# Kernel tuning notes

Hardware: AMD Instinct MI355X
Metric: run time of the kernel (lower is better)

The kernel has to match this reference:

```python
import jax, jax.numpy as jnp
import numpy as np
from functools import partial

V_TH = 1.0
V_RESET = 0.0
ALPHA = 2.0
PI_H = 1.5707963267948966  # pi/2


@jax.custom_vjp
def _spike(v):
    # Heaviside spike with arctan surrogate gradient
    return (v >= V_TH).astype(v.dtype)


def _spike_fwd(v):
    return _spike(v), v - V_TH  # save h = v - V_TH


def _spike_bwd(h, g):
    pah = PI_H * ALPHA * h
    sg = ALPHA / (2.0 * (1.0 + pah * pah))
    return (g * sg,)


_spike.defvjp(_spike_fwd, _spike_bwd)


def _lif_dual(x, decay):
    # x: [T, B, N, C]; decay: [1] broadcast over all elements
    d = decay[0]

    def step(v, xt):
        v = d * v + xt                      # charge: [B, N, C]
        vpool = jnp.mean(v, axis=1)         # spatial mean -> [B, C] (pre-reset v)
        s = _spike(v)
        sr = jax.lax.stop_gradient(s)       # detach_reset=True
        v = (1.0 - sr) * v + sr * V_RESET   # hard reset
        return v, (s, vpool)

    v0 = jnp.zeros_like(x[0])
    _, (spikes, vpool) = jax.lax.scan(step, v0, x)
    return spikes, vpool                    # [T,B,N,C], [T,B,C]


def setup_inputs() -> dict:
    key = jax.random.key(0)
    T, B, N, C = 16, 32, 196, 512
    x = jax.random.normal(key, (T, B, N, C), dtype=jnp.float32)
    # decay = 1 - sigmoid(-log(tau-1)) = 1 - 1/tau = 0.5 for tau=2
    decay = jnp.full((1,), 0.5, dtype=jnp.float32)
    return {"x": x, "decay": decay}


def reference(x, decay):
    return _lif_dual(x, decay)
```

## Files before the change

kernel.cpp:

```cpp
#include <hip/hip_runtime.h>

constexpr int T   = 16;
constexpr int B   = 32;
constexpr int N   = 196;
constexpr int C   = 512;
constexpr int C4  = C / 4;
constexpr int TX  = 64;
constexpr int TY  = 4;
constexpr int RPT = 7;
constexpr int NCHUNK = N / (TY * RPT);
constexpr int CCHUNK = C4 / TX;

__global__ __launch_bounds__(TX * TY) void lif_dual_kernel(
    const float4* __restrict__ x,
    const float*  __restrict__ decay,
    float4* __restrict__ spikes,
    float*  __restrict__ vpool) {
  __shared__ float4 red[TY][4][TX];

  const int tx = threadIdx.x;
  const int ty = threadIdx.y;
  const int cc = blockIdx.x;
  const int nc = blockIdx.y;
  const int b  = blockIdx.z;

  const int c4    = cc * TX + tx;
  const int nbase = nc * (TY * RPT) + ty * RPT;

  const float d     = decay[0];
  const float inv_n = 1.0f / (float)N;

  float4 vpsum[T];
#pragma unroll
  for (int t = 0; t < T; ++t) vpsum[t] = make_float4(0.f, 0.f, 0.f, 0.f);

  const size_t tstride = (size_t)B * N * C4;

#pragma unroll 1
  for (int r = 0; r < RPT; ++r) {
    const int n = nbase + r;
    size_t idx = ((size_t)b * N + n) * C4 + c4;
    float4 v = make_float4(0.f, 0.f, 0.f, 0.f);

#pragma unroll
    for (int t = 0; t < T; ++t) {
      float4 xt = x[idx];

      v.x = d * v.x + xt.x;
      v.y = d * v.y + xt.y;
      v.z = d * v.z + xt.z;
      v.w = d * v.w + xt.w;

      vpsum[t].x += v.x;
      vpsum[t].y += v.y;
      vpsum[t].z += v.z;
      vpsum[t].w += v.w;

      float4 s;
      s.x = (v.x >= 1.0f) ? 1.0f : 0.0f;  v.x = (v.x >= 1.0f) ? 0.0f : v.x;
      s.y = (v.y >= 1.0f) ? 1.0f : 0.0f;  v.y = (v.y >= 1.0f) ? 0.0f : v.y;
      s.z = (v.z >= 1.0f) ? 1.0f : 0.0f;  v.z = (v.z >= 1.0f) ? 0.0f : v.z;
      s.w = (v.w >= 1.0f) ? 1.0f : 0.0f;  v.w = (v.w >= 1.0f) ? 0.0f : v.w;

      spikes[idx] = s;
      idx += tstride;
    }
  }

#pragma unroll 1
  for (int tc = 0; tc < T; tc += 4) {
#pragma unroll
    for (int j = 0; j < 4; ++j) red[ty][j][tx] = vpsum[tc + j];
    __syncthreads();

    float4 a0 = red[0][ty][tx];
    float4 a1 = red[1][ty][tx];
    float4 a2 = red[2][ty][tx];
    float4 a3 = red[3][ty][tx];
    float4 s;
    s.x = (a0.x + a1.x + a2.x + a3.x) * inv_n;
    s.y = (a0.y + a1.y + a2.y + a3.y) * inv_n;
    s.z = (a0.z + a1.z + a2.z + a3.z) * inv_n;
    s.w = (a0.w + a1.w + a2.w + a3.w) * inv_n;

    const int t = tc + ty;
    float* out = vpool + ((size_t)t * B + b) * C + (size_t)c4 * 4;
    atomicAdd(out + 0, s.x);
    atomicAdd(out + 1, s.y);
    atomicAdd(out + 2, s.z);
    atomicAdd(out + 3, s.w);
    __syncthreads();
  }
}

extern "C" void kernel_launch(void* const* d_in, const int* in_sizes, int n_in,
                              void* d_out, int out_size, void* d_ws, size_t ws_size,
                              hipStream_t stream) {
  const float4* x     = (const float4*)d_in[0];
  const float*  decay = (const float*)d_in[1];

  float* out = (float*)d_out;
  const size_t spike_elems = (size_t)T * B * N * C;
  const size_t vpool_elems = (size_t)T * B * C;

  float4* spikes = (float4*)out;
  float*  vpool  = out + spike_elems;

  hipMemsetAsync(vpool, 0, vpool_elems * sizeof(float), stream);

  dim3 block(TX, TY);
  dim3 grid(CCHUNK, NCHUNK, B);
  lif_dual_kernel<<<grid, block, 0, stream>>>(x, decay, spikes, vpool);
}
```

Measured before the change: 391.5 us.

## Replace atomic vpool reduction with partial-sum buffer and second reduction kernel

The float atomicAdd accumulation into vpool (and its memset) is replaced by per-chunk partial sums written to workspace, then reduced by a separate stage-2 kernel. The block shape also changes from 4x7 to 7x2 rows, giving more blocks and threads. Spike outputs are written with nontemporal stores so the large streaming output does not pollute cache. The cost is an extra kernel launch plus workspace traffic for the partial sums, and the result depends on the workspace being large enough.

```diff
diff --git a/kernel.cpp b/kernel.cpp
--- a/kernel.cpp
+++ b/kernel.cpp
@@ -6,16 +6,20 @@
 constexpr int C   = 512;
 constexpr int C4  = C / 4;
 constexpr int TX  = 64;
-constexpr int TY  = 4;
-constexpr int RPT = 7;
-constexpr int NCHUNK = N / (TY * RPT);
+constexpr int TY  = 7;
+constexpr int RPT = 2;
+constexpr int ROWS_PER_BLOCK = TY * RPT;
+constexpr int NCHUNK = N / ROWS_PER_BLOCK;
 constexpr int CCHUNK = C4 / TX;
+constexpr int PCHUNK_F4 = T * B * C4;
 
-__global__ __launch_bounds__(TX * TY) void lif_dual_kernel(
+typedef float f32x4 __attribute__((ext_vector_type(4)));
+
+__global__ __launch_bounds__(TX * TY) void lif_stage1(
     const float4* __restrict__ x,
     const float*  __restrict__ decay,
     float4* __restrict__ spikes,
-    float*  __restrict__ vpool) {
+    float4* __restrict__ partial) {
   __shared__ float4 red[TY][4][TX];
 
   const int tx = threadIdx.x;
@@ -24,11 +28,8 @@
   const int nc = blockIdx.y;
   const int b  = blockIdx.z;
 
-  const int c4    = cc * TX + tx;
-  const int nbase = nc * (TY * RPT) + ty * RPT;
-
-  const float d     = decay[0];
-  const float inv_n = 1.0f / (float)N;
+  const int c4 = cc * TX + tx;
+  const float d = decay[0];
 
   float4 vpsum[T];
 #pragma unroll
@@ -36,9 +37,9 @@
 
   const size_t tstride = (size_t)B * N * C4;
 
-#pragma unroll 1
+#pragma unroll
   for (int r = 0; r < RPT; ++r) {
-    const int n = nbase + r;
+    const int n = nc * ROWS_PER_BLOCK + ty * RPT + r;
     size_t idx = ((size_t)b * N + n) * C4 + c4;
     float4 v = make_float4(0.f, 0.f, 0.f, 0.f);
 
@@ -56,41 +57,54 @@
       vpsum[t].z += v.z;
       vpsum[t].w += v.w;
 
-      float4 s;
+      f32x4 s;
       s.x = (v.x >= 1.0f) ? 1.0f : 0.0f;  v.x = (v.x >= 1.0f) ? 0.0f : v.x;
       s.y = (v.y >= 1.0f) ? 1.0f : 0.0f;  v.y = (v.y >= 1.0f) ? 0.0f : v.y;
       s.z = (v.z >= 1.0f) ? 1.0f : 0.0f;  v.z = (v.z >= 1.0f) ? 0.0f : v.z;
       s.w = (v.w >= 1.0f) ? 1.0f : 0.0f;  v.w = (v.w >= 1.0f) ? 0.0f : v.w;
 
-      spikes[idx] = s;
+      __builtin_nontemporal_store(s, (f32x4*)&spikes[idx]);
       idx += tstride;
     }
   }
 
+  const int flat = ty * TX + tx;
 #pragma unroll 1
   for (int tc = 0; tc < T; tc += 4) {
 #pragma unroll
     for (int j = 0; j < 4; ++j) red[ty][j][tx] = vpsum[tc + j];
     __syncthreads();
-
-    float4 a0 = red[0][ty][tx];
-    float4 a1 = red[1][ty][tx];
-    float4 a2 = red[2][ty][tx];
-    float4 a3 = red[3][ty][tx];
-    float4 s;
-    s.x = (a0.x + a1.x + a2.x + a3.x) * inv_n;
-    s.y = (a0.y + a1.y + a2.y + a3.y) * inv_n;
-    s.z = (a0.z + a1.z + a2.z + a3.z) * inv_n;
-    s.w = (a0.w + a1.w + a2.w + a3.w) * inv_n;
-
-    const int t = tc + ty;
-    float* out = vpool + ((size_t)t * B + b) * C + (size_t)c4 * 4;
-    atomicAdd(out + 0, s.x);
-    atomicAdd(out + 1, s.y);
-    atomicAdd(out + 2, s.z);
-    atomicAdd(out + 3, s.w);
+    if (flat < 4 * TX) {
+      const int j   = flat >> 6;
+      const int col = flat & 63;
+      float4 a = red[0][j][col];
+#pragma unroll
+      for (int k = 1; k < TY; ++k) {
+        float4 r2 = red[k][j][col];
+        a.x += r2.x; a.y += r2.y; a.z += r2.z; a.w += r2.w;
+      }
+      const int t = tc + j;
+      const size_t pidx = (size_t)nc * PCHUNK_F4 +
+                          ((size_t)t * B + b) * C4 + (cc * TX + col);
+      partial[pidx] = a;
+    }
     __syncthreads();
   }
+}
+
+__global__ __launch_bounds__(256) void lif_stage2(
+    const float4* __restrict__ partial,
+    float4* __restrict__ vpool) {
+  const int gid = blockIdx.x * 256 + threadIdx.x;
+  const float inv_n = 1.0f / (float)N;
+  float4 a = partial[gid];
+#pragma unroll
+  for (int k = 1; k < NCHUNK; ++k) {
+    float4 r = partial[(size_t)k * PCHUNK_F4 + gid];
+    a.x += r.x; a.y += r.y; a.z += r.z; a.w += r.w;
+  }
+  a.x *= inv_n; a.y *= inv_n; a.z *= inv_n; a.w *= inv_n;
+  vpool[gid] = a;
 }
 
 extern "C" void kernel_launch(void* const* d_in, const int* in_sizes, int n_in,
@@ -101,14 +115,14 @@
 
   float* out = (float*)d_out;
   const size_t spike_elems = (size_t)T * B * N * C;
-  const size_t vpool_elems = (size_t)T * B * C;
 
-  float4* spikes = (float4*)out;
-  float*  vpool  = out + spike_elems;
+  float4* spikes  = (float4*)out;
+  float4* vpool   = (float4*)(out + spike_elems);
+  float4* partial = (float4*)d_ws;
 
-  hipMemsetAsync(vpool, 0, vpool_elems * sizeof(float), stream);
+  dim3 block1(TX, TY);
+  dim3 grid1(CCHUNK, NCHUNK, B);
+  lif_stage1<<<grid1, block1, 0, stream>>>(x, decay, spikes, partial);
 
-  dim3 block(TX, TY);
-  dim3 grid(CCHUNK, NCHUNK, B);
-  lif_dual_kernel<<<grid, block, 0, stream>>>(x, decay, spikes, vpool);
+  lif_stage2<<<dim3(PCHUNK_F4 / 256), dim3(256), 0, stream>>>(partial, vpool);
 }
```

Measured after the change: 434.4 us. 1.11x slower.
